# Kernel optimization log

Hardware: AMD Instinct MI355X
Metric: run time of the kernel (lower is better)

Reference implementation:

```python
import jax, jax.numpy as jnp
import numpy as np

B, S, D, H = 4, 2048, 1024, 16
DK = D // H
NEG = -1e9  # stand-in for -inf; keeps softmax grads NaN-free, same math after softmax


def setup_inputs() -> dict:
    key = jax.random.key(0)
    ks = jax.random.split(key, 8)
    scale = 0.02
    return {
        "q": jax.random.normal(ks[0], (B, S, D), jnp.float32),
        "k": jax.random.normal(ks[1], (B, S, D), jnp.float32),
        "v": jax.random.normal(ks[2], (B, S, D), jnp.float32),
        "mask": jnp.ones((B, S), jnp.int32),
        "Wq": jax.random.normal(ks[3], (D, D), jnp.float32) * scale,
        "bq": jnp.zeros((D,), jnp.float32),
        "Wk": jax.random.normal(ks[4], (D, D), jnp.float32) * scale,
        "bk": jnp.zeros((D,), jnp.float32),
        "Wv": jax.random.normal(ks[5], (D, D), jnp.float32) * scale,
        "bv": jnp.zeros((D,), jnp.float32),
        "Wp": jax.random.normal(ks[6], (D, D), jnp.float32) * scale,
        "bp": jnp.zeros((D,), jnp.float32),
    }


def reference(q, k, v, mask, Wq, bq, Wk, bk, Wv, bv, Wp, bp):
    # torch.nn.Linear: y = x @ W.T + b
    Q = q @ Wq.T + bq  # [B,S,D]
    K = k @ Wk.T + bk
    V = v @ Wv.T + bv
    # split heads -> [B,H,S,dk]
    Q = Q.reshape(B, S, H, DK).transpose(0, 2, 1, 3)
    K = K.reshape(B, S, H, DK).transpose(0, 2, 1, 3)
    V = V.reshape(B, S, H, DK).transpose(0, 2, 1, 3)
    Sc = jnp.einsum("bhqd,bhkd->bhqk", Q, K) / jnp.sqrt(jnp.float32(DK))
    # padding mask: [B,1,1,Sk]
    Sc = jnp.where(mask[:, None, None, :] == 0, NEG, Sc)
    # causal mask (tril), as in the registered buffer
    causal = jnp.tril(jnp.ones((S, S), jnp.bool_))
    Sc = jnp.where(causal, Sc, NEG)
    A = jax.nn.softmax(Sc, axis=-1)  # attn_drop with p=0 is identity
    x = jnp.einsum("bhqk,bhkd->bhqd", A, V)
    x = x.transpose(0, 2, 1, 3).reshape(B, S, D)
    return x @ Wp.T + bp
```

## Files before the change

### kernel.cpp

```cpp
#include <hip/hip_runtime.h>
#include <stdint.h>


#define SZB (8192u * 1024u * 2u)
#define WSZ (1024u * 1024u * 2u)
#define NKT 16
#define SLOT 24576

typedef __attribute__((ext_vector_type(8))) short  short8;
typedef __attribute__((ext_vector_type(4))) short  short4v;
typedef __attribute__((ext_vector_type(4))) float  f32x4;

#define MFMA16(a, b, c) __builtin_amdgcn_mfma_f32_16x16x32_bf16(a, b, c, 0, 0, 0)

__device__ __forceinline__ f32x4 mfma_k16(short4v a, short4v b, f32x4 c) {
#if __has_builtin(__builtin_amdgcn_mfma_f32_16x16x16bf16_1k)
  return __builtin_amdgcn_mfma_f32_16x16x16bf16_1k(a, b, c, 0, 0, 0);
#else
  asm volatile("v_mfma_f32_16x16x16_bf16 %0, %1, %2, %0"
               : "+v"(c) : "v"(a), "v"(b));
  return c;
#endif
}
__device__ __forceinline__ uint32_t cvtpk(float a, float b) {
  uint32_t r;
  asm("v_cvt_pk_bf16_f32 %0, %1, %2" : "=v"(r) : "v"(a), "v"(b));
  return r;
}

__device__ __forceinline__ ushort f2bf(float f) {
  uint32_t u = __float_as_uint(f);
  u += 0x7FFF + ((u >> 16) & 1);
  return (ushort)(u >> 16);
}
__device__ __forceinline__ short8 cvt8(float4 a, float4 b) {
  short8 r;
  r[0] = (short)f2bf(a.x); r[1] = (short)f2bf(a.y);
  r[2] = (short)f2bf(a.z); r[3] = (short)f2bf(a.w);
  r[4] = (short)f2bf(b.x); r[5] = (short)f2bf(b.y);
  r[6] = (short)f2bf(b.z); r[7] = (short)f2bf(b.w);
  return r;
}
__device__ __forceinline__ void gl_lds16(const ushort* g, ushort* l) {
  __builtin_amdgcn_global_load_lds(
      (__attribute__((address_space(1))) void*)g,
      (__attribute__((address_space(3))) void*)l, 16, 0, 0);
}

__global__ __launch_bounds__(256) void cvt_all(
    const float* __restrict__ q, const float* __restrict__ k,
    const float* __restrict__ v,
    const float* __restrict__ Wq, const float* __restrict__ Wk,
    const float* __restrict__ Wv, const float* __restrict__ Wp,
    ushort* __restrict__ qb2, ushort* __restrict__ kb2,
    ushort* __restrict__ vb2,
    ushort* __restrict__ Wqb, ushort* __restrict__ Wkb,
    ushort* __restrict__ Wvb, ushort* __restrict__ Wpb) {
  const int z = blockIdx.y;
  const bool big = (z == 0) | (z == 1) | (z == 6);
  if (!big && blockIdx.x >= 512) return;
  const float* s = (z == 0) ? q   : (z == 1) ? k   : (z == 2) ? Wq :
                   (z == 3) ? Wk  : (z == 4) ? Wv  : (z == 5) ? Wp : v;
  ushort* d      = (z == 0) ? qb2 : (z == 1) ? kb2 : (z == 2) ? Wqb :
                   (z == 3) ? Wkb : (z == 4) ? Wvb : (z == 5) ? Wpb : vb2;
  const size_t i = (size_t)(blockIdx.x * 256 + threadIdx.x) * 8;
  *(short8*)&d[i] = cvt8(*(const float4*)&s[i], *(const float4*)&s[i + 4]);
}

__device__ __forceinline__ void core8p(
    const ushort* __restrict__ A, const ushort* __restrict__ Wb,
    ushort* lds, int m0, int n0, f32x4 acc[4][4]) {
  const int tid  = threadIdx.x;
  const int w    = tid >> 6;
  const int lane = tid & 63;
  const int quad = lane >> 4;
  const int l16  = lane & 15;
  const int wm   = (w >> 1) * 64;
  const int wn   = (w & 1) * 64;

  const ushort* asrc[4];
  const ushort* bsrc[2];
#pragma unroll
  for (int i = 0; i < 4; ++i) {
    const int c = tid + 512 * i;
    asrc[i] = A + (size_t)(m0 + (c >> 3)) * 1024 + ((c & 7) ^ ((c >> 3) & 7)) * 8;
  }
#pragma unroll
  for (int i = 0; i < 2; ++i) {
    const int c = tid + 512 * i;
    bsrc[i] = Wb + (size_t)(n0 + (c >> 3)) * 1024 + ((c & 7) ^ ((c >> 3) & 7)) * 8;
  }

  auto stage = [&](int j, int s) {
    ushort* base = lds + s * SLOT + w * 512;
#pragma unroll
    for (int i = 0; i < 4; ++i)
      gl_lds16(asrc[i] + j * 64, base + i * 4096);
#pragma unroll
    for (int i = 0; i < 2; ++i)
      gl_lds16(bsrc[i] + j * 64, base + 16384 + i * 4096);
  };

  const int rsw = (l16 & 7) * 8;
  auto compute = [&](int s) {
    const ushort* pA = lds + s * SLOT;
    const ushort* pB = pA + 16384;
    short8 a[4][2], b[4][2];
#pragma unroll
    for (int f = 0; f < 4; ++f)
#pragma unroll
      for (int ks = 0; ks < 2; ++ks) {
        a[f][ks] = *(const short8*)&pA[(wm + f * 16 + l16) * 64 +
                                       ((ks * 32 + quad * 8) ^ rsw)];
        b[f][ks] = *(const short8*)&pB[(wn + f * 16 + l16) * 64 +
                                       ((ks * 32 + quad * 8) ^ rsw)];
      }
    __builtin_amdgcn_s_setprio(1);
#pragma unroll
    for (int i = 0; i < 4; ++i)
#pragma unroll
      for (int j2 = 0; j2 < 4; ++j2) {
        acc[i][j2] = MFMA16(a[i][0], b[j2][0], acc[i][j2]);
        acc[i][j2] = MFMA16(a[i][1], b[j2][1], acc[i][j2]);
      }
    __builtin_amdgcn_s_setprio(0);
  };

  stage(0, 0);
  stage(1, 1);
  int s = 0;
#pragma unroll 1
  for (int j = 0; j < NKT - 1; ++j) {
    asm volatile("s_waitcnt vmcnt(6)" ::: "memory");
    __builtin_amdgcn_s_barrier();
    __builtin_amdgcn_sched_barrier(0);
    if (j < NKT - 2) {
      int s2 = s + 2; if (s2 >= 3) s2 -= 3;
      stage(j + 2, s2);
    }
    compute(s);
    if (++s == 3) s = 0;
  }
  asm volatile("s_waitcnt vmcnt(0)" ::: "memory");
  __builtin_amdgcn_s_barrier();
  __builtin_amdgcn_sched_barrier(0);
  compute(s);
}

__device__ __forceinline__ void xcd_map(int& m0, int& n0) {
  const int x = (int)blockIdx.x;
  m0 = ((x & 7) * 4 + (x >> 3)) * 256;
  n0 = (int)blockIdx.y * 128;
}

__global__ __launch_bounds__(512, 2) void gemm_qkv8(
    const ushort* __restrict__ qb2, const ushort* __restrict__ kb2,
    const ushort* __restrict__ vb2,
    const ushort* __restrict__ Wqb, const ushort* __restrict__ Wkb,
    const ushort* __restrict__ Wvb,
    const float* __restrict__ bq, const float* __restrict__ bk,
    const float* __restrict__ bv,
    ushort* __restrict__ Qb, ushort* __restrict__ Kb, ushort* __restrict__ Vt) {
  __shared__ ushort lds[3 * SLOT];

  const int z = blockIdx.z;
  const ushort* A    = (z == 0) ? qb2 : (z == 1) ? kb2 : vb2;
  const ushort* W    = (z == 0) ? Wqb : (z == 1) ? Wkb : Wvb;
  const float*  bias = (z == 0) ? bq  : (z == 1) ? bk  : bv;

  int m0, n0;
  xcd_map(m0, n0);

  f32x4 acc[4][4] = {};
  core8p(A, W, lds, m0, n0, acc);

  const int tid  = threadIdx.x;
  const int w    = tid >> 6;
  const int lane = tid & 63;
  const int quad = lane >> 4;
  const int l16  = lane & 15;
  const int wm   = (w >> 1) * 64;
  const int wn   = (w & 1) * 64;

  float bvv[4];
#pragma unroll
  for (int j = 0; j < 4; ++j) bvv[j] = bias[n0 + wn + j * 16 + l16];

  if (z < 2) {
    ushort* Out = (z == 0) ? Qb : Kb;
    const float sc = (z == 0) ? 0.1803368801f : 1.0f;
#pragma unroll
    for (int i = 0; i < 4; ++i) {
      const int m = m0 + wm + i * 16 + quad * 4;
#pragma unroll
      for (int j = 0; j < 4; ++j) {
        const int n = n0 + wn + j * 16 + l16;
#pragma unroll
        for (int r = 0; r < 4; ++r)
          Out[(size_t)(m + r) * 1024 + n] = f2bf((acc[i][j][r] + bvv[j]) * sc);
      }
    }
  } else {
#pragma unroll
    for (int i = 0; i < 4; ++i) {
      const int mrow = m0 + wm + i * 16 + quad * 4;
      const int bb   = mrow >> 11;
      const int s0   = mrow & 2047;
#pragma unroll
      for (int j = 0; j < 4; ++j) {
        const int n = n0 + wn + j * 16 + l16;
        ushort4 pk;
        pk.x = f2bf(acc[i][j][0] + bvv[j]);
        pk.y = f2bf(acc[i][j][1] + bvv[j]);
        pk.z = f2bf(acc[i][j][2] + bvv[j]);
        pk.w = f2bf(acc[i][j][3] + bvv[j]);
        *(ushort4*)&Vt[(size_t)((bb * 16 + (n >> 6)) * 64 + (n & 63)) * 2048 + s0] = pk;
      }
    }
  }
}

__global__ __launch_bounds__(512, 2) void gemm_proj8(
    const ushort* __restrict__ Xin, const ushort* __restrict__ Wpb,
    const float* __restrict__ bp, float* __restrict__ Out) {
  __shared__ ushort lds[3 * SLOT];

  int m0, n0;
  xcd_map(m0, n0);

  f32x4 acc[4][4] = {};
  core8p(Xin, Wpb, lds, m0, n0, acc);

  const int tid  = threadIdx.x;
  const int w    = tid >> 6;
  const int lane = tid & 63;
  const int quad = lane >> 4;
  const int l16  = lane & 15;
  const int wm   = (w >> 1) * 64;
  const int wn   = (w & 1) * 64;

  float bvv[4];
#pragma unroll
  for (int j = 0; j < 4; ++j) bvv[j] = bp[n0 + wn + j * 16 + l16];

#pragma unroll
  for (int i = 0; i < 4; ++i) {
    const int m = m0 + wm + i * 16 + quad * 4;
#pragma unroll
    for (int j = 0; j < 4; ++j) {
      const int n = n0 + wn + j * 16 + l16;
#pragma unroll
      for (int r = 0; r < 4; ++r)
        Out[(size_t)(m + r) * 1024 + n] = acc[i][j][r] + bvv[j];
    }
  }
}

__global__ __launch_bounds__(256) void gemm_v_fb(
    const float* __restrict__ vin, const ushort* __restrict__ Wvb,
    const float* __restrict__ bv, ushort* __restrict__ Vt) {
  __shared__ ushort As[128 * 32];
  __shared__ ushort Bs[128 * 32];

  const int tid  = threadIdx.x;
  const int w    = tid >> 6;
  const int lane = tid & 63;
  const int quad = lane >> 4;
  const int l16  = lane & 15;
  const int wm   = (w >> 1) * 64;
  const int wn   = (w & 1) * 64;
  const int r0   = tid >> 2;
  const int r1   = r0 + 64;
  const int c0   = (tid & 3) * 8;

  const int m0 = blockIdx.x * 128;
  const int n0 = blockIdx.y * 128;

  f32x4 acc[4][4] = {};
  const ushort* Wg = Wvb + (size_t)(n0 + w * 32 + (lane >> 2)) * 1024 + (lane & 3) * 8;
  const float*  Ag0 = vin + (size_t)(m0 + r0) * 1024 + c0;
  const float*  Ag1 = vin + (size_t)(m0 + r1) * 1024 + c0;

  float4 p0a = *(const float4*)(Ag0), p0b = *(const float4*)(Ag0 + 4);
  float4 p1a = *(const float4*)(Ag1), p1b = *(const float4*)(Ag1 + 4);

  for (int kt = 0; kt < 32; ++kt) {
    const int ko = kt * 32;
    __syncthreads();
    *(short8*)&As[r0 * 32 + c0] = cvt8(p0a, p0b);
    *(short8*)&As[r1 * 32 + c0] = cvt8(p1a, p1b);
    gl_lds16(Wg + ko,         &Bs[(w * 32) * 32]);
    gl_lds16(Wg + 16384 + ko, &Bs[(w * 32 + 16) * 32]);
    __syncthreads();
    if (kt < 31) {
      const int kn = ko + 32;
      p0a = *(const float4*)(Ag0 + kn); p0b = *(const float4*)(Ag0 + kn + 4);
      p1a = *(const float4*)(Ag1 + kn); p1b = *(const float4*)(Ag1 + kn + 4);
    }
    short8 af[4], bfr[4];
#pragma unroll
    for (int i = 0; i < 4; ++i)
      af[i] = *(const short8*)&As[(wm + i * 16 + l16) * 32 + quad * 8];
#pragma unroll
    for (int i = 0; i < 4; ++i)
      bfr[i] = *(const short8*)&Bs[(wn + i * 16 + l16) * 32 + quad * 8];
#pragma unroll
    for (int i = 0; i < 4; ++i)
#pragma unroll
      for (int j = 0; j < 4; ++j)
        acc[i][j] = MFMA16(af[i], bfr[j], acc[i][j]);
  }

  float bvv[4];
#pragma unroll
  for (int j = 0; j < 4; ++j) bvv[j] = bv[n0 + wn + j * 16 + l16];
#pragma unroll
  for (int i = 0; i < 4; ++i) {
    const int mrow = m0 + wm + i * 16 + quad * 4;
    const int bb   = mrow >> 11;
    const int s0   = mrow & 2047;
#pragma unroll
    for (int j = 0; j < 4; ++j) {
      const int n = n0 + wn + j * 16 + l16;
      ushort4 pk;
      pk.x = f2bf(acc[i][j][0] + bvv[j]);
      pk.y = f2bf(acc[i][j][1] + bvv[j]);
      pk.z = f2bf(acc[i][j][2] + bvv[j]);
      pk.w = f2bf(acc[i][j][3] + bvv[j]);
      *(ushort4*)&Vt[(size_t)((bb * 16 + (n >> 6)) * 64 + (n & 63)) * 2048 + s0] = pk;
    }
  }
}

__global__ __launch_bounds__(256, 4) void attn(
    ushort* __restrict__ Qb, const ushort* __restrict__ Kb,
    const ushort* __restrict__ Vt, const int* __restrict__ mask) {
  __shared__ ushort Ks[64 * 68];
  __shared__ ushort Vts[64 * 68];

  const int wgid = (int)blockIdx.x + 16 * (int)blockIdx.y;
  const int xcd  = wgid & 7;
  const int idx  = wgid >> 3;
  const int bh   = xcd * 8 + (idx >> 4);
  const int pair = idx & 15;
  const int b = bh >> 4, h = bh & 15;
  const int tid = threadIdx.x, w = tid >> 6, lane = tid & 63;
  const int quad = lane >> 4, l16 = lane & 15;
  const int ql = w * 16 + l16;

  short8 kst[2], vst[2];
  int mld;

  auto ld_tile = [&](int k0) {
#pragma unroll
    for (int i = 0; i < 2; ++i) {
      const int c = tid + 256 * i;
      kst[i] = *(const short8*)&Kb[(size_t)(b * 2048 + k0 + (c >> 3)) * 1024 +
                                   h * 64 + (c & 7) * 8];
      vst[i] = *(const short8*)&Vt[(size_t)(bh * 64 + (c >> 3)) * 2048 +
                                   k0 + (c & 7) * 8];
    }
    mld = mask[b * 2048 + k0 + lane];
  };

#pragma unroll 1
  for (int seg = 0; seg < 2; ++seg) {
    const int qt = seg ? (31 - pair) : pair;
    const int q0 = qt * 64;

    const size_t qoff = (size_t)(b * 2048 + q0 + w * 16 + l16) * 1024 + h * 64 + quad * 8;
    const short8 qf0 = *(const short8*)&Qb[qoff];
    const short8 qf1 = *(const short8*)&Qb[qoff + 32];

    f32x4 oacc[4] = {};
    float lsum[4] = {0.f, 0.f, 0.f, 0.f};

    ld_tile(0);

    for (int kt = 0; kt <= qt; ++kt) {
      __syncthreads();
#pragma unroll
      for (int i = 0; i < 2; ++i) {
        const int c = tid + 256 * i;
        *(short8*)&Ks[(c >> 3) * 68 + (c & 7) * 8]  = kst[i];
        *(short8*)&Vts[(c >> 3) * 68 + (c & 7) * 8] = vst[i];
      }
      const int mcur = mld;
      __syncthreads();

      if (kt < qt) ld_tile((kt + 1) * 64);

      const unsigned long long mbits = __ballot(mcur != 0);
      const bool allm = (mbits == ~0ull);

      f32x4 sc[4];
#pragma unroll
      for (int nj = 0; nj < 4; ++nj) {
        f32x4 z4 = {0.f, 0.f, 0.f, 0.f};
        const short8 kf0 = *(const short8*)&Ks[(nj * 16 + l16) * 68 + quad * 8];
        const short8 kf1 = *(const short8*)&Ks[(nj * 16 + l16) * 68 + 32 + quad * 8];
        z4 = MFMA16(kf0, qf0, z4);
        z4 = MFMA16(kf1, qf1, z4);
        sc[nj] = z4;
      }

      float pv[4][4];
      if (kt < qt) {
        if (allm) {
#pragma unroll
          for (int nj = 0; nj < 4; ++nj)
#pragma unroll
            for (int r = 0; r < 4; ++r)
              pv[nj][r] = __builtin_amdgcn_exp2f(sc[nj][r]);
        } else {
#pragma unroll
          for (int nj = 0; nj < 4; ++nj) {
            const uint32_t sub = (uint32_t)(mbits >> (nj * 16));
#pragma unroll
            for (int r = 0; r < 4; ++r) {
              const bool ok = (sub >> (quad * 4 + r)) & 1;
              pv[nj][r] = __builtin_amdgcn_exp2f(ok ? sc[nj][r] : -1e5f);
            }
          }
        }
      } else {
#pragma unroll
        for (int nj = 0; nj < 4; ++nj) {
          const uint32_t sub = allm ? 0xffffffffu : (uint32_t)(mbits >> (nj * 16));
#pragma unroll
          for (int r = 0; r < 4; ++r) {
            const int kl = nj * 16 + quad * 4 + r;
            const bool ok = ((sub >> (quad * 4 + r)) & 1) && (kl <= ql);
            pv[nj][r] = __builtin_amdgcn_exp2f(ok ? sc[nj][r] : -1e5f);
          }
        }
      }
#pragma unroll
      for (int nj = 0; nj < 4; ++nj)
#pragma unroll
        for (int r = 0; r < 4; ++r) lsum[r] += pv[nj][r];

      short4v pa[4];
#pragma unroll
      for (int nj = 0; nj < 4; ++nj) {
        uint32_t u0 = cvtpk(pv[nj][0], pv[nj][1]);
        uint32_t u1 = cvtpk(pv[nj][2], pv[nj][3]);
        pa[nj][0] = (short)(u0 & 0xffff); pa[nj][1] = (short)(u0 >> 16);
        pa[nj][2] = (short)(u1 & 0xffff); pa[nj][3] = (short)(u1 >> 16);
      }

#pragma unroll
      for (int nj = 0; nj < 4; ++nj)
#pragma unroll
        for (int nb = 0; nb < 4; ++nb) {
          const short4v vf = *(const short4v*)&Vts[(nb * 16 + l16) * 68 +
                                                   nj * 16 + quad * 4];
          oacc[nb] = mfma_k16(pa[nj], vf, oacc[nb]);
        }
    }

    float v = lsum[0] + lsum[1] + lsum[2] + lsum[3];
    v += __shfl_xor(v, 16);
    v += __shfl_xor(v, 32);
    const float inv = 1.0f / v;
    float invr[4];
#pragma unroll
    for (int r = 0; r < 4; ++r) invr[r] = __shfl(inv, quad * 4 + r);

#pragma unroll
    for (int nb = 0; nb < 4; ++nb)
#pragma unroll
      for (int r = 0; r < 4; ++r) {
        const int q = q0 + w * 16 + quad * 4 + r;
        Qb[(size_t)(b * 2048 + q) * 1024 + h * 64 + nb * 16 + l16] =
            f2bf(oacc[nb][r] * invr[r]);
      }
  }
}

extern "C" void kernel_launch(void* const* d_in, const int* in_sizes, int n_in,
                              void* d_out, int out_size, void* d_ws, size_t ws_size,
                              hipStream_t stream) {
  const float* q    = (const float*)d_in[0];
  const float* k    = (const float*)d_in[1];
  const float* v    = (const float*)d_in[2];
  const int*   mask = (const int*)d_in[3];
  const float* Wq   = (const float*)d_in[4];
  const float* bq   = (const float*)d_in[5];
  const float* Wk   = (const float*)d_in[6];
  const float* bk   = (const float*)d_in[7];
  const float* Wv   = (const float*)d_in[8];
  const float* bv   = (const float*)d_in[9];
  const float* Wp   = (const float*)d_in[10];
  const float* bp   = (const float*)d_in[11];
  float* out = (float*)d_out;

  char* ws = (char*)d_ws;
  ushort* Qb  = (ushort*)(ws);
  ushort* Kb  = (ushort*)(ws + (size_t)SZB);
  ushort* Vt  = (ushort*)(ws + (size_t)2 * SZB);
  ushort* Wqb = (ushort*)(ws + (size_t)3 * SZB);
  ushort* Wkb = (ushort*)(ws + (size_t)3 * SZB + WSZ);
  ushort* Wvb = (ushort*)(ws + (size_t)3 * SZB + 2 * WSZ);
  ushort* Wpb = (ushort*)(ws + (size_t)3 * SZB + 3 * WSZ);

  ushort* qb2 = (ushort*)out;
  ushort* kb2 = (ushort*)((char*)out + (size_t)SZB);
  const size_t need_v = (size_t)3 * SZB + 4 * WSZ + SZB;
  const int v_bf = (ws_size >= need_v) ? 1 : 0;
  ushort* vb2 = v_bf ? (ushort*)(ws + (size_t)3 * SZB + 4 * WSZ) : nullptr;

  cvt_all<<<dim3(4096, 6 + v_bf), dim3(256), 0, stream>>>(
      q, k, v, Wq, Wk, Wv, Wp, qb2, kb2, vb2, Wqb, Wkb, Wvb, Wpb);
  gemm_qkv8<<<dim3(32, 8, 2 + v_bf), dim3(512), 0, stream>>>(
      qb2, kb2, vb2, Wqb, Wkb, Wvb, bq, bk, bv, Qb, Kb, Vt);
  if (!v_bf)
    gemm_v_fb<<<dim3(64, 8), dim3(256), 0, stream>>>(v, Wvb, bv, Vt);
  attn<<<dim3(16, 64), dim3(256), 0, stream>>>(Qb, Kb, Vt, mask);
  gemm_proj8<<<dim3(32, 8), dim3(512), 0, stream>>>(Qb, Wpb, bp, out);
}
```

Measured before the change: 298.4 us.

## Double-buffer K/V shared-memory tiles in attention to drop one barrier per step

Gives the K and V^T shared tiles two buffers. Tile kt+1 is written to LDS while tile kt is being computed, and the global prefetch runs two tiles ahead. This cuts the two __syncthreads per key tile down to one and overlaps LDS stores with MFMA work. It also replaces the manual bf16 packing with a bit_cast. In exchange, LDS use per block doubles (about 35 KB), which may limit occupancy at 4 blocks per CU, and more registers stay live.

```diff
diff --git a/kernel.cpp b/kernel.cpp
--- a/kernel.cpp
+++ b/kernel.cpp
@@ -10,6 +10,7 @@
 typedef __attribute__((ext_vector_type(8))) short  short8;
 typedef __attribute__((ext_vector_type(4))) short  short4v;
 typedef __attribute__((ext_vector_type(4))) float  f32x4;
+typedef __attribute__((ext_vector_type(2))) uint32_t uint2v;
 
 #define MFMA16(a, b, c) __builtin_amdgcn_mfma_f32_16x16x32_bf16(a, b, c, 0, 0, 0)
 
@@ -335,8 +336,8 @@
 __global__ __launch_bounds__(256, 4) void attn(
     ushort* __restrict__ Qb, const ushort* __restrict__ Kb,
     const ushort* __restrict__ Vt, const int* __restrict__ mask) {
-  __shared__ ushort Ks[64 * 68];
-  __shared__ ushort Vts[64 * 68];
+  __shared__ ushort Ks[2][64 * 68];
+  __shared__ ushort Vts[2][64 * 68];
 
   const int wgid = (int)blockIdx.x + 16 * (int)blockIdx.y;
   const int xcd  = wgid & 7;
@@ -348,6 +349,9 @@
   const int quad = lane >> 4, l16 = lane & 15;
   const int ql = w * 16 + l16;
 
+  const int c0r = tid >> 3, c0c = (tid & 7) * 8;
+  const int c1r = (tid + 256) >> 3, c1c = ((tid + 256) & 7) * 8;
+
   short8 kst[2], vst[2];
   int mld;
 
@@ -362,6 +366,12 @@
     }
     mld = mask[b * 2048 + k0 + lane];
   };
+  auto wr_tile = [&](int buf) {
+    *(short8*)&Ks[buf][c0r * 68 + c0c]  = kst[0];
+    *(short8*)&Vts[buf][c0r * 68 + c0c] = vst[0];
+    *(short8*)&Ks[buf][c1r * 68 + c1c]  = kst[1];
+    *(short8*)&Vts[buf][c1r * 68 + c1c] = vst[1];
+  };
 
 #pragma unroll 1
   for (int seg = 0; seg < 2; ++seg) {
@@ -376,29 +386,31 @@
     float lsum[4] = {0.f, 0.f, 0.f, 0.f};
 
     ld_tile(0);
+    __syncthreads();
+    wr_tile(0);
+    int mcur = mld;
+    if (qt > 0) ld_tile(64);
 
     for (int kt = 0; kt <= qt; ++kt) {
       __syncthreads();
-#pragma unroll
-      for (int i = 0; i < 2; ++i) {
-        const int c = tid + 256 * i;
-        *(short8*)&Ks[(c >> 3) * 68 + (c & 7) * 8]  = kst[i];
-        *(short8*)&Vts[(c >> 3) * 68 + (c & 7) * 8] = vst[i];
-      }
-      const int mcur = mld;
-      __syncthreads();
-
-      if (kt < qt) ld_tile((kt + 1) * 64);
-
-      const unsigned long long mbits = __ballot(mcur != 0);
+      const int mthis = mcur;
+      if (kt < qt) {
+        wr_tile((kt + 1) & 1);
+        mcur = mld;
+        if (kt + 1 < qt) ld_tile((kt + 2) * 64);
+      }
+      const ushort* Kc = Ks[kt & 1];
+      const ushort* Vc = Vts[kt & 1];
+
+      const unsigned long long mbits = __ballot(mthis != 0);
       const bool allm = (mbits == ~0ull);
 
       f32x4 sc[4];
 #pragma unroll
       for (int nj = 0; nj < 4; ++nj) {
         f32x4 z4 = {0.f, 0.f, 0.f, 0.f};
-        const short8 kf0 = *(const short8*)&Ks[(nj * 16 + l16) * 68 + quad * 8];
-        const short8 kf1 = *(const short8*)&Ks[(nj * 16 + l16) * 68 + 32 + quad * 8];
+        const short8 kf0 = *(const short8*)&Kc[(nj * 16 + l16) * 68 + quad * 8];
+        const short8 kf1 = *(const short8*)&Kc[(nj * 16 + l16) * 68 + 32 + quad * 8];
         z4 = MFMA16(kf0, qf0, z4);
         z4 = MFMA16(kf1, qf1, z4);
         sc[nj] = z4;
@@ -443,18 +455,18 @@
       short4v pa[4];
 #pragma unroll
       for (int nj = 0; nj < 4; ++nj) {
-        uint32_t u0 = cvtpk(pv[nj][0], pv[nj][1]);
-        uint32_t u1 = cvtpk(pv[nj][2], pv[nj][3]);
-        pa[nj][0] = (short)(u0 & 0xffff); pa[nj][1] = (short)(u0 >> 16);
-        pa[nj][2] = (short)(u1 & 0xffff); pa[nj][3] = (short)(u1 >> 16);
+        uint2v uu;
+        uu[0] = cvtpk(pv[nj][0], pv[nj][1]);
+        uu[1] = cvtpk(pv[nj][2], pv[nj][3]);
+        pa[nj] = __builtin_bit_cast(short4v, uu);
       }
 
 #pragma unroll
       for (int nj = 0; nj < 4; ++nj)
 #pragma unroll
         for (int nb = 0; nb < 4; ++nb) {
-          const short4v vf = *(const short4v*)&Vts[(nb * 16 + l16) * 68 +
-                                                   nj * 16 + quad * 4];
+          const short4v vf = *(const short4v*)&Vc[(nb * 16 + l16) * 68 +
+                                                  nj * 16 + quad * 4];
           oacc[nb] = mfma_k16(pa[nj], vf, oacc[nb]);
         }
     }
```

After: 388.5 us. 30.2% more time.
